# Optimization experiments

Hardware: AMD Instinct MI355X
Metric: run time of the kernel (lower is better)

## Reference

```python
import jax, jax.numpy as jnp
import numpy as np

WIN = 8          # window side -> N = 64 tokens per window
HEADS = 8
NCAV = 2
EGO_DIST_BINS = 4
EGO_ANGLE_BINS = 4


def _rel_pos_index(wh, ww):
    # Swin-style relative position index, (wh*ww, wh*ww) int
    coords = np.stack(np.meshgrid(np.arange(wh), np.arange(ww), indexing='ij'))  # (2,wh,ww)
    flat = coords.reshape(2, -1)
    rel = (flat[:, :, None] - flat[:, None, :]).transpose(1, 2, 0).astype(np.int64)
    rel[:, :, 0] += wh - 1
    rel[:, :, 1] += ww - 1
    rel[:, :, 0] *= 2 * ww - 1
    return jnp.asarray(rel.sum(-1))


def _ego_bias_index(affine_matrix, H, W):
    # per-(cav,window) bin index into ego_position_bias_table
    gy, gx = jnp.meshgrid(jnp.arange(H // WIN), jnp.arange(W // WIN), indexing='ij')
    centers = jnp.stack([gx * WIN + WIN / 2.0, gy * WIN + WIN / 2.0], axis=-1)
    centers = centers.reshape(-1, 2).astype(jnp.float32)              # (nW, 2)
    img_c = jnp.array([[W / 2.0], [H / 2.0]], jnp.float32)            # (2, 1)
    ego = (affine_matrix[:, :2, :2] @ img_c + affine_matrix[:, :2, 2:3])[..., 0]  # (ncav, 2)
    rel = centers[None, :, :] - ego[:, None, :]                        # (ncav, nW, 2)
    dist = jnp.linalg.norm(rel, axis=-1)
    ang = jnp.arctan2(rel[..., 1], rel[..., 0])
    db = (dist / (dist.max() + 1e-6) * (EGO_DIST_BINS - 1)).astype(jnp.int32)
    ab = ((ang + jnp.pi) / (2 * jnp.pi) * (EGO_ANGLE_BINS - 1)).astype(jnp.int32)
    return (db * EGO_ANGLE_BINS + ab).reshape(-1)                      # (ncav*nW,) == (B_,)


def setup_inputs() -> dict:
    key = jax.random.key(0)
    ks = jax.random.split(key, 10)
    H = W = 256
    B_ = NCAV * (H // WIN) * (W // WIN)   # 2048
    N = WIN * WIN                          # 64
    C = 256
    s = 0.02
    return {
        'x': jax.random.normal(ks[0], (B_, N, C), jnp.float32),
        'affine_matrix': jax.random.normal(ks[1], (NCAV, 2, 3), jnp.float32),
        'Wq': jax.random.normal(ks[2], (C, C), jnp.float32) * s,
        'bq': jax.random.normal(ks[3], (C,), jnp.float32) * s,
        'Wkv': jax.random.normal(ks[4], (C, 2 * C), jnp.float32) * s,
        'bkv': jax.random.normal(ks[5], (2 * C,), jnp.float32) * s,
        'Wp': jax.random.normal(ks[6], (C, C), jnp.float32) * s,
        'bp': jax.random.normal(ks[7], (C,), jnp.float32) * s,
        'rel_table': jax.random.normal(ks[8], ((2 * WIN - 1) ** 2, HEADS), jnp.float32) * s,
        'ego_table': jax.random.normal(ks[9], (EGO_DIST_BINS * EGO_ANGLE_BINS, HEADS), jnp.float32) * s,
        'w': jnp.ones((2,), jnp.float32),
        'H': H,
        'W': W,
    }


def reference(x, affine_matrix, Wq, bq, Wkv, bkv, Wp, bp, rel_table, ego_table, w, H, W):
    B_, N, C = x.shape
    h = HEADS
    hd = C // h
    scale = hd ** -0.5

    q = (x @ Wq + bq).reshape(B_, N, h, hd).transpose(0, 2, 1, 3)          # (B_, h, N, hd)
    kv = (x @ Wkv + bkv).reshape(B_, N, 2, h, hd).transpose(2, 0, 3, 1, 4)
    k, v = kv[0], kv[1]                                                     # (B_, h, N, hd)

    attn = jnp.einsum('bhnd,bhmd->bhnm', q * scale, k)                      # (B_, h, N, N)

    # Swin relative position bias
    rpi = _rel_pos_index(WIN, WIN)
    rel_bias = rel_table[rpi.reshape(-1)].reshape(N, N, h).transpose(2, 0, 1)  # (h, N, N)

    # ego-relative bias: one scalar per (window, head), broadcast over NxN
    idx = _ego_bias_index(affine_matrix, H, W)                              # (B_,)
    ego_bias = ego_table[idx]                                               # (B_, h)

    attn = attn + rel_bias[None, :, :, :] + ego_bias[:, :, None, None]

    attn0 = jax.nn.softmax(attn, axis=-1)
    attn1 = jnp.square(jnp.maximum(attn, 0.0))   # relu(attn)**2 (no-mask branch)
    ws = jax.nn.softmax(w)
    attn = attn0 * ws[0] + attn1 * ws[1]

    out = jnp.einsum('bhnm,bhmd->bhnd', attn, v).transpose(0, 2, 1, 3).reshape(B_, N, C)
    return out @ Wp + bp
```

## Files before the change

kernel.cpp:

```cpp
#include <hip/hip_runtime.h>

#define NWIN 2048
#define NT   64
#define CDIM 256
#define NHEAD 8
#define HD   32
#define SCALE 0.17677669529663687f

typedef short bfrag __attribute__((ext_vector_type(8)));
typedef float f4    __attribute__((ext_vector_type(4)));
typedef unsigned short us4 __attribute__((ext_vector_type(4)));

__device__ __forceinline__ unsigned short f2bf(float f){
  unsigned u = __builtin_bit_cast(unsigned, f);
  u += 0x7FFFu + ((u >> 16) & 1u);
  return (unsigned short)(u >> 16);
}

__device__ __forceinline__ f4 mfma16(bfrag a, bfrag b, f4 c){
  return __builtin_amdgcn_mfma_f32_16x16x32_bf16(a, b, c, 0, 0, 0);
}

__global__ void prep_kernel(const float* __restrict__ aff,
                            const float* __restrict__ Wq,  const float* __restrict__ bq,
                            const float* __restrict__ Wkv, const float* __restrict__ bkv,
                            const float* __restrict__ Wp,
                            const float* __restrict__ relt, const float* __restrict__ egot,
                            unsigned short* __restrict__ wt, float* __restrict__ relb,
                            float* __restrict__ egob, float* __restrict__ bqkv)
{
  const int bid = blockIdx.x, tid = threadIdx.x;
  if (bid < 1024) {
    int r = bid, c = tid;
    float v;
    if (r < 256)      v = Wq[c*256 + r] * SCALE;
    else if (r < 768) v = Wkv[c*512 + (r - 256)];
    else              v = Wp[c*256 + (r - 768)];
    wt[r*256 + c] = f2bf(v);
  } else if (bid < 1152) {
    int e = (bid - 1024)*256 + tid;
    int h = e >> 12, i = (e >> 6) & 63, j = e & 63;
    int yi = i >> 3, xi = i & 7, yj = j >> 3, xj = j & 7;
    int ridx = (yi - yj + 7)*15 + (xi - xj + 7);
    relb[e] = relt[ridx*8 + h];
  } else if (bid == 1152) {
    __shared__ float red[256];
    float ex[2], ey[2];
    for (int cv = 0; cv < 2; ++cv){
      const float* A = aff + cv*6;
      ex[cv] = (A[0] + A[1])*128.0f + A[2];
      ey[cv] = (A[3] + A[4])*128.0f + A[5];
    }
    float dl = 0.0f;
    for (int p = 0; p < 4; ++p){
      int t = p*256 + tid;
      float cx = (float)((t & 31)*8 + 4), cy = (float)((t >> 5)*8 + 4);
      for (int cv = 0; cv < 2; ++cv){
        float dx = cx - ex[cv], dy = cy - ey[cv];
        dl = fmaxf(dl, sqrtf(dx*dx + dy*dy));
      }
    }
    red[tid] = dl; __syncthreads();
    for (int s = 128; s > 0; s >>= 1){
      if (tid < s) red[tid] = fmaxf(red[tid], red[tid + s]);
      __syncthreads();
    }
    float dmax = red[0] + 1e-6f;
    const float PI_F = 3.14159265358979f;
    for (int p = 0; p < 4; ++p){
      int t = p*256 + tid;
      float cx = (float)((t & 31)*8 + 4), cy = (float)((t >> 5)*8 + 4);
      for (int cv = 0; cv < 2; ++cv){
        float dx = cx - ex[cv], dy = cy - ey[cv];
        float d = sqrtf(dx*dx + dy*dy);
        float ang = atan2f(dy, dx);
        int db = (int)(d / dmax * 3.0f);
        int ab = (int)((ang + PI_F) / (2.0f*PI_F) * 3.0f);
        int idx = db*4 + ab;
        int bw = cv*1024 + t;
        for (int h2 = 0; h2 < 8; ++h2)
          egob[bw*8 + h2] = egot[idx*8 + h2];
      }
    }
  } else {
    for (int j = tid; j < 768; j += 256)
      bqkv[j] = (j < 256) ? bq[j]*SCALE : bkv[j - 256];
  }
}

__global__ __launch_bounds__(1024) void attn_kernel(
    const float* __restrict__ x, const float* __restrict__ wvec,
    const float* __restrict__ bp, float* __restrict__ out,
    const unsigned short* __restrict__ wt, const float* __restrict__ relb,
    const float* __restrict__ egob, const float* __restrict__ bqkv)
{
  __shared__ unsigned short lds_x[NT*CDIM];
  __shared__ unsigned short lds_qkv[NHEAD*6144];

  const int b = blockIdx.x;
  const int tid = threadIdx.x;
  const int wv = tid >> 6, lane = tid & 63;
  const int quad = lane >> 4, cc = lane & 15;

  const float4* xg = (const float4*)(x + (size_t)b*(NT*CDIM));
  for (int it = 0; it < 4; ++it){
    int i4 = tid + it*1024;
    float4 v = xg[i4];
    us4 pk = { f2bf(v.x), f2bf(v.y), f2bf(v.z), f2bf(v.w) };
    *(us4*)(&lds_x[i4*4]) = pk;
  }
  float w0 = wvec[0], w1 = wvec[1];
  float wm = fmaxf(w0, w1);
  float e0 = __expf(w0 - wm), e1 = __expf(w1 - wm);
  float ws0 = e0/(e0+e1), ws1 = e1/(e0+e1);
  __syncthreads();

  {
    const int ob = wv*48;
    f4 acc[3][4];
    for (int mt=0;mt<3;++mt) for (int nt=0;nt<4;++nt) acc[mt][nt] = (f4){0,0,0,0};
    for (int ks = 0; ks < 8; ++ks){
      bfrag afr[3], bfr[4];
      for (int mt=0;mt<3;++mt)
        afr[mt] = *(const bfrag*)(wt + (ob + mt*16 + cc)*256 + ks*32 + quad*8);
      for (int nt=0;nt<4;++nt)
        bfr[nt] = *(const bfrag*)(&lds_x[(nt*16 + cc)*256 + ks*32 + quad*8]);
      for (int mt=0;mt<3;++mt)
        for (int nt=0;nt<4;++nt)
          acc[mt][nt] = mfma16(afr[mt], bfr[nt], acc[mt][nt]);
    }
    for (int mt=0;mt<3;++mt){
      int oc0 = ob + mt*16 + quad*4;
      float bb0 = bqkv[oc0], bb1 = bqkv[oc0+1], bb2 = bqkv[oc0+2], bb3 = bqkv[oc0+3];
      int part = oc0 >> 8, ch = oc0 & 255;
      int h2 = ch >> 5, d0 = ch & 31;
      unsigned short* slab = &lds_qkv[h2*6144 + part*2048];
      for (int nt=0;nt<4;++nt){
        int tok = nt*16 + cc;
        float v0 = acc[mt][nt][0] + bb0;
        float v1 = acc[mt][nt][1] + bb1;
        float v2 = acc[mt][nt][2] + bb2;
        float v3 = acc[mt][nt][3] + bb3;
        if (part < 2){
          us4 pk = { f2bf(v0), f2bf(v1), f2bf(v2), f2bf(v3) };
          *(us4*)(&slab[tok*32 + d0]) = pk;
        } else {
          slab[(d0+0)*64 + tok] = f2bf(v0);
          slab[(d0+1)*64 + tok] = f2bf(v1);
          slab[(d0+2)*64 + tok] = f2bf(v2);
          slab[(d0+3)*64 + tok] = f2bf(v3);
        }
      }
    }
  }
  __syncthreads();

  const int h = wv >> 1, half = wv & 1;
  f4 yacc[2][2];
  {
    const unsigned short* qs  = &lds_qkv[h*6144];
    const unsigned short* ks_ = qs + 2048;
    const unsigned short* vts = qs + 4096;
    float ego = egob[b*8 + h];
    const float* rb = relb + h*4096;

    bfrag bk[4];
    for (int jt=0;jt<4;++jt)
      bk[jt] = *(const bfrag*)(&ks_[(jt*16 + cc)*32 + quad*8]);
    f4 S[2][4];
    for (int it=0;it<2;++it){
      bfrag aq = *(const bfrag*)(&qs[(half*32 + it*16 + cc)*32 + quad*8]);
      for (int jt=0;jt<4;++jt){
        f4 z = (f4){0,0,0,0};
        S[it][jt] = mfma16(aq, bk[jt], z);
      }
    }
    float a[2][4][4];
    for (int it=0;it<2;++it)
      for (int jt=0;jt<4;++jt){
        int jj = jt*16 + cc;
        for (int r=0;r<4;++r){
          int ii = half*32 + it*16 + quad*4 + r;
          a[it][r][jt] = S[it][jt][r] + rb[ii*64 + jj] + ego;
        }
      }
    float rmax[2][4], rinv[2][4];
    for (int it=0;it<2;++it)
      for (int r=0;r<4;++r){
        float m = fmaxf(fmaxf(a[it][r][0], a[it][r][1]), fmaxf(a[it][r][2], a[it][r][3]));
        for (int off=1; off<16; off<<=1) m = fmaxf(m, __shfl_xor(m, off, 64));
        float s = 0.0f;
        for (int jt=0;jt<4;++jt) s += __expf(a[it][r][jt] - m);
        for (int off=1; off<16; off<<=1) s += __shfl_xor(s, off, 64);
        rmax[it][r] = m; rinv[it][r] = 1.0f / s;
      }
    for (int it=0;it<2;++it) for (int nt=0;nt<2;++nt) yacc[it][nt] = (f4){0,0,0,0};
    unsigned short* Pw = &lds_x[wv*1024];
    for (int chunk=0; chunk<2; ++chunk){
      for (int it=0;it<2;++it)
        for (int jtl=0;jtl<2;++jtl){
          int jt = chunk*2 + jtl;
          for (int r=0;r<4;++r){
            float av = a[it][r][jt];
            float rl = fmaxf(av, 0.0f);
            float p = ws0 * __expf(av - rmax[it][r]) * rinv[it][r] + ws1 * rl * rl;
            Pw[(it*16 + quad*4 + r)*32 + jtl*16 + cc] = f2bf(p);
          }
        }
      bfrag pa[2], pb[2];
      for (int itl=0;itl<2;++itl)
        pa[itl] = *(const bfrag*)(&Pw[(itl*16 + cc)*32 + quad*8]);
      for (int nt=0;nt<2;++nt)
        pb[nt] = *(const bfrag*)(&vts[(nt*16 + cc)*64 + chunk*32 + quad*8]);
      for (int itl=0;itl<2;++itl)
        for (int nt=0;nt<2;++nt)
          yacc[itl][nt] = mfma16(pa[itl], pb[nt], yacc[itl][nt]);
    }
  }
  __syncthreads();
  for (int itl=0;itl<2;++itl)
    for (int nt=0;nt<2;++nt)
      for (int r=0;r<4;++r){
        int ii = half*32 + itl*16 + quad*4 + r;
        lds_x[ii*256 + h*32 + nt*16 + cc] = f2bf(yacc[itl][nt][r]);
      }
  __syncthreads();

  {
    const int mt = wv & 3;
    const int cb = (wv >> 2)*64;
    f4 o[4];
    for (int nt=0;nt<4;++nt) o[nt] = (f4){0,0,0,0};
    for (int ks=0; ks<8; ++ks){
      bfrag ay = *(const bfrag*)(&lds_x[(mt*16 + cc)*256 + ks*32 + quad*8]);
      for (int nt=0;nt<4;++nt){
        bfrag bw = *(const bfrag*)(wt + (768 + cb + nt*16 + cc)*256 + ks*32 + quad*8);
        o[nt] = mfma16(ay, bw, o[nt]);
      }
    }
    float* og = out + (size_t)b*(NT*CDIM);
    for (int nt=0;nt<4;++nt){
      int col = cb + nt*16 + cc;
      float bpv = bp[col];
      for (int r=0;r<4;++r){
        int tok = mt*16 + quad*4 + r;
        og[tok*256 + col] = o[nt][r] + bpv;
      }
    }
  }
}

extern "C" void kernel_launch(void* const* d_in, const int* in_sizes, int n_in,
                              void* d_out, int out_size, void* d_ws, size_t ws_size,
                              hipStream_t stream)
{
  const float* x    = (const float*)d_in[0];
  const float* aff  = (const float*)d_in[1];
  const float* Wq   = (const float*)d_in[2];
  const float* bq   = (const float*)d_in[3];
  const float* Wkv  = (const float*)d_in[4];
  const float* bkv  = (const float*)d_in[5];
  const float* Wp   = (const float*)d_in[6];
  const float* bp   = (const float*)d_in[7];
  const float* relt = (const float*)d_in[8];
  const float* egot = (const float*)d_in[9];
  const float* w    = (const float*)d_in[10];
  float* out = (float*)d_out;

  char* ws = (char*)d_ws;
  unsigned short* wt = (unsigned short*)ws;
  float* relb = (float*)(ws + 524288);
  float* egob = (float*)(ws + 655360);
  float* bqkv = (float*)(ws + 720896);

  hipLaunchKernelGGL(prep_kernel, dim3(1154), dim3(256), 0, stream,
                     aff, Wq, bq, Wkv, bkv, Wp, relt, egot, wt, relb, egob, bqkv);
  hipLaunchKernelGGL(attn_kernel, dim3(2048), dim3(1024), 0, stream,
                     x, w, bp, out, wt, relb, egob, bqkv);
}
```

Before: 513.7 us.

## Swizzle LDS layouts, pad Q/K rows, prefetch weight fragments, tile weight transpose

XOR-swizzles the shared-memory layouts for x, V-transpose, P and the attention output, and pads Q/K rows to a stride of 40, to cut LDS bank conflicts on the MFMA fragment loads. It also software-prefetches the next k-step's global weight fragments in both GEMMs, and rewrites the prep weight transpose as 32x32 shared-memory tiles so global accesses coalesce. The launch bounds now request 4 blocks per CU. Costs are extra register pressure from the prefetch buffers, larger LDS use from the padding, and more index arithmetic.

Result: no change. 515.7 us (+0.4%).

```diff
diff --git a/kernel.cpp b/kernel.cpp
--- a/kernel.cpp
+++ b/kernel.cpp
@@ -20,6 +20,8 @@
 __device__ __forceinline__ f4 mfma16(bfrag a, bfrag b, f4 c){
   return __builtin_amdgcn_mfma_f32_16x16x32_bf16(a, b, c, 0, 0, 0);
 }
+
+__device__ __forceinline__ int swx(int row, int u){ return (row << 5) + (u ^ (row & 7)); }
 
 __global__ void prep_kernel(const float* __restrict__ aff,
                             const float* __restrict__ Wq,  const float* __restrict__ bq,
@@ -30,20 +32,31 @@
                             float* __restrict__ egob, float* __restrict__ bqkv)
 {
   const int bid = blockIdx.x, tid = threadIdx.x;
-  if (bid < 1024) {
-    int r = bid, c = tid;
-    float v;
-    if (r < 256)      v = Wq[c*256 + r] * SCALE;
-    else if (r < 768) v = Wkv[c*512 + (r - 256)];
-    else              v = Wp[c*256 + (r - 768)];
-    wt[r*256 + c] = f2bf(v);
-  } else if (bid < 1152) {
-    int e = (bid - 1024)*256 + tid;
+  if (bid < 256) {
+    __shared__ float t[32][33];
+    const int r0 = (bid >> 3) * 32;
+    const int c0 = (bid & 7) * 32;
+    const int rl = tid & 31, ch = tid >> 5;
+    for (int k = 0; k < 4; ++k){
+      int c = c0 + ch + k*8, r = r0 + rl;
+      float v;
+      if (r < 256)      v = Wq[c*256 + r] * SCALE;
+      else if (r < 768) v = Wkv[c*512 + (r - 256)];
+      else              v = Wp[c*256 + (r - 768)];
+      t[rl][ch + k*8] = v;
+    }
+    __syncthreads();
+    for (int k = 0; k < 4; ++k){
+      int orr = ch + k*8;
+      wt[(r0 + orr)*256 + c0 + rl] = f2bf(t[orr][rl]);
+    }
+  } else if (bid < 384) {
+    int e = (bid - 256)*256 + tid;
     int h = e >> 12, i = (e >> 6) & 63, j = e & 63;
     int yi = i >> 3, xi = i & 7, yj = j >> 3, xj = j & 7;
     int ridx = (yi - yj + 7)*15 + (xi - xj + 7);
     relb[e] = relt[ridx*8 + h];
-  } else if (bid == 1152) {
+  } else if (bid == 384) {
     __shared__ float red[256];
     float ex[2], ey[2];
     for (int cv = 0; cv < 2; ++cv){
@@ -53,8 +66,8 @@
     }
     float dl = 0.0f;
     for (int p = 0; p < 4; ++p){
-      int t = p*256 + tid;
-      float cx = (float)((t & 31)*8 + 4), cy = (float)((t >> 5)*8 + 4);
+      int t2 = p*256 + tid;
+      float cx = (float)((t2 & 31)*8 + 4), cy = (float)((t2 >> 5)*8 + 4);
       for (int cv = 0; cv < 2; ++cv){
         float dx = cx - ex[cv], dy = cy - ey[cv];
         dl = fmaxf(dl, sqrtf(dx*dx + dy*dy));
@@ -68,8 +81,8 @@
     float dmax = red[0] + 1e-6f;
     const float PI_F = 3.14159265358979f;
     for (int p = 0; p < 4; ++p){
-      int t = p*256 + tid;
-      float cx = (float)((t & 31)*8 + 4), cy = (float)((t >> 5)*8 + 4);
+      int t2 = p*256 + tid;
+      float cx = (float)((t2 & 31)*8 + 4), cy = (float)((t2 >> 5)*8 + 4);
       for (int cv = 0; cv < 2; ++cv){
         float dx = cx - ex[cv], dy = cy - ey[cv];
         float d = sqrtf(dx*dx + dy*dy);
@@ -77,7 +90,7 @@
         int db = (int)(d / dmax * 3.0f);
         int ab = (int)((ang + PI_F) / (2.0f*PI_F) * 3.0f);
         int idx = db*4 + ab;
-        int bw = cv*1024 + t;
+        int bw = cv*1024 + t2;
         for (int h2 = 0; h2 < 8; ++h2)
           egob[bw*8 + h2] = egot[idx*8 + h2];
       }
@@ -88,14 +101,17 @@
   }
 }
 
-__global__ __launch_bounds__(1024) void attn_kernel(
+#define QK_LD 40
+#define HSLAB 7168
+
+__global__ __launch_bounds__(1024, 4) void attn_kernel(
     const float* __restrict__ x, const float* __restrict__ wvec,
     const float* __restrict__ bp, float* __restrict__ out,
     const unsigned short* __restrict__ wt, const float* __restrict__ relb,
     const float* __restrict__ egob, const float* __restrict__ bqkv)
 {
   __shared__ unsigned short lds_x[NT*CDIM];
-  __shared__ unsigned short lds_qkv[NHEAD*6144];
+  __shared__ unsigned short lds_qkv[NHEAD*HSLAB];
 
   const int b = blockIdx.x;
   const int tid = threadIdx.x;
@@ -107,7 +123,8 @@
     int i4 = tid + it*1024;
     float4 v = xg[i4];
     us4 pk = { f2bf(v.x), f2bf(v.y), f2bf(v.z), f2bf(v.w) };
-    *(us4*)(&lds_x[i4*4]) = pk;
+    int row = i4 >> 6, u = (i4 & 63) >> 1, hf = i4 & 1;
+    *(us4*)(&lds_x[swx(row, u)*8 + hf*4]) = pk;
   }
   float w0 = wvec[0], w1 = wvec[1];
   float wm = fmaxf(w0, w1);
@@ -119,22 +136,29 @@
     const int ob = wv*48;
     f4 acc[3][4];
     for (int mt=0;mt<3;++mt) for (int nt=0;nt<4;++nt) acc[mt][nt] = (f4){0,0,0,0};
+    bfrag afr[3], nafr[3];
+    for (int mt=0;mt<3;++mt)
+      afr[mt] = *(const bfrag*)(wt + (ob + mt*16 + cc)*256 + quad*8);
+    #pragma unroll
     for (int ks = 0; ks < 8; ++ks){
-      bfrag afr[3], bfr[4];
-      for (int mt=0;mt<3;++mt)
-        afr[mt] = *(const bfrag*)(wt + (ob + mt*16 + cc)*256 + ks*32 + quad*8);
+      if (ks < 7)
+        for (int mt=0;mt<3;++mt)
+          nafr[mt] = *(const bfrag*)(wt + (ob + mt*16 + cc)*256 + (ks+1)*32 + quad*8);
+      bfrag bfr[4];
       for (int nt=0;nt<4;++nt)
-        bfr[nt] = *(const bfrag*)(&lds_x[(nt*16 + cc)*256 + ks*32 + quad*8]);
+        bfr[nt] = *(const bfrag*)(&lds_x[swx(nt*16 + cc, ks*4 + quad)*8]);
       for (int mt=0;mt<3;++mt)
         for (int nt=0;nt<4;++nt)
           acc[mt][nt] = mfma16(afr[mt], bfr[nt], acc[mt][nt]);
+      if (ks < 7)
+        for (int mt=0;mt<3;++mt) afr[mt] = nafr[mt];
     }
     for (int mt=0;mt<3;++mt){
       int oc0 = ob + mt*16 + quad*4;
       float bb0 = bqkv[oc0], bb1 = bqkv[oc0+1], bb2 = bqkv[oc0+2], bb3 = bqkv[oc0+3];
       int part = oc0 >> 8, ch = oc0 & 255;
       int h2 = ch >> 5, d0 = ch & 31;
-      unsigned short* slab = &lds_qkv[h2*6144 + part*2048];
+      unsigned short* hb = &lds_qkv[h2*HSLAB];
       for (int nt=0;nt<4;++nt){
         int tok = nt*16 + cc;
         float v0 = acc[mt][nt][0] + bb0;
@@ -143,12 +167,14 @@
         float v3 = acc[mt][nt][3] + bb3;
         if (part < 2){
           us4 pk = { f2bf(v0), f2bf(v1), f2bf(v2), f2bf(v3) };
-          *(us4*)(&slab[tok*32 + d0]) = pk;
+          *(us4*)(&hb[part*2560 + tok*QK_LD + d0]) = pk;
         } else {
-          slab[(d0+0)*64 + tok] = f2bf(v0);
-          slab[(d0+1)*64 + tok] = f2bf(v1);
-          slab[(d0+2)*64 + tok] = f2bf(v2);
-          slab[(d0+3)*64 + tok] = f2bf(v3);
+          unsigned short* vs = hb + 5120;
+          int tu = tok >> 3, te = tok & 7;
+          vs[(d0+0)*64 + ((tu ^ ((d0+0)&7))<<3) + te] = f2bf(v0);
+          vs[(d0+1)*64 + ((tu ^ ((d0+1)&7))<<3) + te] = f2bf(v1);
+          vs[(d0+2)*64 + ((tu ^ ((d0+2)&7))<<3) + te] = f2bf(v2);
+          vs[(d0+3)*64 + ((tu ^ ((d0+3)&7))<<3) + te] = f2bf(v3);
         }
       }
     }
@@ -158,18 +184,18 @@
   const int h = wv >> 1, half = wv & 1;
   f4 yacc[2][2];
   {
-    const unsigned short* qs  = &lds_qkv[h*6144];
-    const unsigned short* ks_ = qs + 2048;
-    const unsigned short* vts = qs + 4096;
+    const unsigned short* qs  = &lds_qkv[h*HSLAB];
+    const unsigned short* ks_ = qs + 2560;
+    const unsigned short* vts = qs + 5120;
     float ego = egob[b*8 + h];
     const float* rb = relb + h*4096;
 
     bfrag bk[4];
     for (int jt=0;jt<4;++jt)
-      bk[jt] = *(const bfrag*)(&ks_[(jt*16 + cc)*32 + quad*8]);
+      bk[jt] = *(const bfrag*)(&ks_[(jt*16 + cc)*QK_LD + quad*8]);
     f4 S[2][4];
     for (int it=0;it<2;++it){
-      bfrag aq = *(const bfrag*)(&qs[(half*32 + it*16 + cc)*32 + quad*8]);
+      bfrag aq = *(const bfrag*)(&qs[(half*32 + it*16 + cc)*QK_LD + quad*8]);
       for (int jt=0;jt<4;++jt){
         f4 z = (f4){0,0,0,0};
         S[it][jt] = mfma16(aq, bk[jt], z);
@@ -204,14 +230,19 @@
             float av = a[it][r][jt];
             float rl = fmaxf(av, 0.0f);
             float p = ws0 * __expf(av - rmax[it][r]) * rinv[it][r] + ws1 * rl * rl;
-            Pw[(it*16 + quad*4 + r)*32 + jtl*16 + cc] = f2bf(p);
+            int row = it*16 + quad*4 + r, col = jtl*16 + cc;
+            Pw[row*32 + (((col>>3) ^ (row&3))<<3) + (col&7)] = f2bf(p);
           }
         }
       bfrag pa[2], pb[2];
-      for (int itl=0;itl<2;++itl)
-        pa[itl] = *(const bfrag*)(&Pw[(itl*16 + cc)*32 + quad*8]);
-      for (int nt=0;nt<2;++nt)
-        pb[nt] = *(const bfrag*)(&vts[(nt*16 + cc)*64 + chunk*32 + quad*8]);
+      for (int itl=0;itl<2;++itl){
+        int row = itl*16 + cc;
+        pa[itl] = *(const bfrag*)(&Pw[row*32 + ((quad ^ (row&3))<<3)]);
+      }
+      for (int nt=0;nt<2;++nt){
+        int row = nt*16 + cc;
+        pb[nt] = *(const bfrag*)(&vts[row*64 + (((chunk*4 + quad) ^ (row&7))<<3)]);
+      }
       for (int itl=0;itl<2;++itl)
         for (int nt=0;nt<2;++nt)
           yacc[itl][nt] = mfma16(pa[itl], pb[nt], yacc[itl][nt]);
@@ -222,7 +253,8 @@
     for (int nt=0;nt<2;++nt)
       for (int r=0;r<4;++r){
         int ii = half*32 + itl*16 + quad*4 + r;
-        lds_x[ii*256 + h*32 + nt*16 + cc] = f2bf(yacc[itl][nt][r]);
+        int col = h*32 + nt*16 + cc;
+        lds_x[swx(ii, col>>3)*8 + (col&7)] = f2bf(yacc[itl][nt][r]);
       }
   __syncthreads();
 
@@ -231,12 +263,19 @@
     const int cb = (wv >> 2)*64;
     f4 o[4];
     for (int nt=0;nt<4;++nt) o[nt] = (f4){0,0,0,0};
+    bfrag bw[4], nbw[4];
+    for (int nt=0;nt<4;++nt)
+      bw[nt] = *(const bfrag*)(wt + (768 + cb + nt*16 + cc)*256 + quad*8);
+    #pragma unroll
     for (int ks=0; ks<8; ++ks){
-      bfrag ay = *(const bfrag*)(&lds_x[(mt*16 + cc)*256 + ks*32 + quad*8]);
-      for (int nt=0;nt<4;++nt){
-        bfrag bw = *(const bfrag*)(wt + (768 + cb + nt*16 + cc)*256 + ks*32 + quad*8);
-        o[nt] = mfma16(ay, bw, o[nt]);
-      }
+      if (ks < 7)
+        for (int nt=0;nt<4;++nt)
+          nbw[nt] = *(const bfrag*)(wt + (768 + cb + nt*16 + cc)*256 + (ks+1)*32 + quad*8);
+      bfrag ay = *(const bfrag*)(&lds_x[swx(mt*16 + cc, ks*4 + quad)*8]);
+      for (int nt=0;nt<4;++nt)
+        o[nt] = mfma16(ay, bw[nt], o[nt]);
+      if (ks < 7)
+        for (int nt=0;nt<4;++nt) bw[nt] = nbw[nt];
     }
     float* og = out + (size_t)b*(NT*CDIM);
     for (int nt=0;nt<4;++nt){
@@ -273,7 +312,7 @@
   float* egob = (float*)(ws + 655360);
   float* bqkv = (float*)(ws + 720896);
 
-  hipLaunchKernelGGL(prep_kernel, dim3(1154), dim3(256), 0, stream,
+  hipLaunchKernelGGL(prep_kernel, dim3(386), dim3(256), 0, stream,
                      aff, Wq, bq, Wkv, bkv, Wp, relt, egot, wt, relb, egob, bqkv);
   hipLaunchKernelGGL(attn_kernel, dim3(2048), dim3(1024), 0, stream,
                      x, w, bp, out, wt, relb, egob, bqkv);
```
